# Kernel tuning notes

Hardware: AMD Instinct MI355X
Metric: run time of the kernel (lower is better)

## Reference

```python
import jax, jax.numpy as jnp
import numpy as np


def setup_inputs() -> dict:
    key = jax.random.key(0)
    k1, k2 = jax.random.split(key)
    preds = jax.random.normal(k1, (16, 4096, 3), dtype=jnp.float32)
    gts = jax.random.normal(k2, (16, 4096, 3), dtype=jnp.float32)
    return {"preds": preds, "gts": gts}


def _pairwise_sqdist(x, y):
    # x: [B, N1, D], y: [B, N2, D] -> P: [B, N1, N2]
    rx = jnp.sum(x * x, axis=-1)  # [B, N1]
    ry = jnp.sum(y * y, axis=-1)  # [B, N2]
    zz = jnp.einsum("bnd,bmd->bnm", x, y)  # [B, N1, N2]
    return rx[:, :, None] + ry[:, None, :] - 2.0 * zz


def reference(preds, gts):
    # Symmetric Hausdorff distance (squared-dist version) per batch element.
    P = _pairwise_sqdist(preds, gts)  # [B, N1, N2]
    # min over preds (axis 1) for each gt point, then max over gt points
    loss1 = jnp.max(jnp.min(P, axis=1), axis=1)  # [B]
    # min over gts (axis 2) for each pred point, then max over pred points
    loss2 = jnp.max(jnp.min(P, axis=2), axis=1)  # [B]
    return (loss1 + loss2) * 0.5
```

## Files before the change

kernel.cpp:

```cpp
#include <hip/hip_runtime.h>
#include <math.h>


#define NPTS 4096
#define NB 16
#define TPB 256
#define M 8
#define SPLIT 16
#define HT (TPB * M)
#define OC (NPTS / SPLIT)
#define NHT (NPTS / HT)

#define WSMIN_N (2 * NB * NPTS)

__global__ __launch_bounds__(TPB) void haus_scan_kernel(
        const float* __restrict__ preds, const float* __restrict__ gts,
        unsigned int* __restrict__ wsmin) {
    const int ht  = blockIdx.x & (NHT - 1);
    const int oc  = blockIdx.x >> 1;
    const int b   = blockIdx.y;
    const int dir = blockIdx.z;
    const int t   = threadIdx.x;

    const float* home = (dir == 0) ? gts : preds;
    const float* opp  = (dir == 0) ? preds : gts;
    const float* hb = home + (size_t)b * NPTS * 3;
    const float* ob = opp  + (size_t)b * NPTS * 3;

    __shared__ float4 q[OC];
    {
        const float* src = ob + (size_t)(oc * OC + t) * 3;
        float qx = src[0], qy = src[1], qz = src[2];
        float hq = 0.5f * fmaf(qx, qx, fmaf(qy, qy, qz * qz));
        q[t] = make_float4(qx, qy, qz, hq);
    }

    float px[M], py[M], pz[M], best[M];
#pragma unroll
    for (int k = 0; k < M; ++k) {
        int hi = ht * HT + k * TPB + t;
        px[k] = hb[hi * 3 + 0];
        py[k] = hb[hi * 3 + 1];
        pz[k] = hb[hi * 3 + 2];
        best[k] = INFINITY;
    }

    __syncthreads();

#pragma unroll 4
    for (int j = 0; j < OC; ++j) {
        float4 q4 = q[j];
        float qx = q4.x, qy = q4.y, qz = q4.z, qw = q4.w;
        asm("" : "+v"(qx), "+v"(qy), "+v"(qz), "+v"(qw));
#pragma unroll
        for (int k = 0; k < M; ++k) {
            float acc = fmaf(-px[k], qx, qw);
            acc = fmaf(-py[k], qy, acc);
            acc = fmaf(-pz[k], qz, acc);
            best[k] = fminf(best[k], acc);
        }
    }

    unsigned int* slot = wsmin + ((size_t)dir * NB + b) * NPTS;
#pragma unroll
    for (int k = 0; k < M; ++k) {
        int hi = ht * HT + k * TPB + t;
        float hp = 0.5f * fmaf(px[k], px[k], fmaf(py[k], py[k], pz[k] * pz[k]));
        float d2 = fmaxf(best[k] + hp, 0.0f);
        atomicMin(slot + hi, __float_as_uint(d2));
    }
}

__global__ __launch_bounds__(TPB) void haus_final_kernel(
        const unsigned int* __restrict__ wsmin, float* __restrict__ out) {
    const int b = blockIdx.x;
    const int t = threadIdx.x;
    const float4* w0 = (const float4*)(wsmin + ((size_t)0 * NB + b) * NPTS);
    const float4* w1 = (const float4*)(wsmin + ((size_t)1 * NB + b) * NPTS);
    float m1 = -INFINITY, m2 = -INFINITY;
#pragma unroll
    for (int r = 0; r < NPTS / 4 / TPB; ++r) {
        float4 a = w0[r * TPB + t];
        float4 c = w1[r * TPB + t];
        m1 = fmaxf(fmaxf(fmaxf(a.x, a.y), fmaxf(a.z, a.w)), m1);
        m2 = fmaxf(fmaxf(fmaxf(c.x, c.y), fmaxf(c.z, c.w)), m2);
    }
#pragma unroll
    for (int off = 32; off > 0; off >>= 1) {
        m1 = fmaxf(m1, __shfl_down(m1, off, 64));
        m2 = fmaxf(m2, __shfl_down(m2, off, 64));
    }
    __shared__ float s1[4], s2[4];
    if ((t & 63) == 0) { s1[t >> 6] = m1; s2[t >> 6] = m2; }
    __syncthreads();
    if (t == 0) {
        float a = fmaxf(fmaxf(s1[0], s1[1]), fmaxf(s1[2], s1[3]));
        float c = fmaxf(fmaxf(s2[0], s2[1]), fmaxf(s2[2], s2[3]));
        out[b] = a + c;
    }
}

extern "C" void kernel_launch(void* const* d_in, const int* in_sizes, int n_in,
                              void* d_out, int out_size, void* d_ws, size_t ws_size,
                              hipStream_t stream) {
    const float* preds = (const float*)d_in[0];
    const float* gts   = (const float*)d_in[1];
    float* out = (float*)d_out;
    unsigned int* wsmin = (unsigned int*)d_ws;

    hipMemsetAsync(wsmin, 0xFF, (size_t)WSMIN_N * sizeof(unsigned int), stream);

    haus_scan_kernel<<<dim3(NHT * SPLIT, NB, 2), dim3(TPB), 0, stream>>>(
        preds, gts, wsmin);

    haus_final_kernel<<<dim3(NB), dim3(TPB), 0, stream>>>(wsmin, out);
}
```

Baseline: 97.54 us.

## Use packed v_pk_fma_f32 and give each thread 16 home points

The inner distance loop now pairs two home points per register and computes their partial distances with v_pk_fma_f32 inline assembly. This cuts the FMA instruction count per pair roughly in half, while the fmin stays scalar. Each thread now holds 16 home points, so one block covers all 4096 points in a batch. The opposite set is split 32 ways with 128 points per block, so each LDS query load is reused across more points. Register use goes up, and the hand-written op_sel encodings must match the intended lane selection.

After: 95.71 us. No clear change (-1.9%).

```diff
diff --git a/kernel.cpp b/kernel.cpp
--- a/kernel.cpp
+++ b/kernel.cpp
@@ -5,19 +5,19 @@
 #define NPTS 4096
 #define NB 16
 #define TPB 256
-#define M 8
-#define SPLIT 16
-#define HT (TPB * M)
+#define M 16
+#define MP (M / 2)
+#define SPLIT 32
 #define OC (NPTS / SPLIT)
-#define NHT (NPTS / HT)
 
 #define WSMIN_N (2 * NB * NPTS)
+
+typedef float v2f __attribute__((ext_vector_type(2)));
 
 __global__ __launch_bounds__(TPB) void haus_scan_kernel(
         const float* __restrict__ preds, const float* __restrict__ gts,
         unsigned int* __restrict__ wsmin) {
-    const int ht  = blockIdx.x & (NHT - 1);
-    const int oc  = blockIdx.x >> 1;
+    const int oc  = blockIdx.x;
     const int b   = blockIdx.y;
     const int dir = blockIdx.z;
     const int t   = threadIdx.x;
@@ -27,47 +27,59 @@
     const float* hb = home + (size_t)b * NPTS * 3;
     const float* ob = opp  + (size_t)b * NPTS * 3;
 
-    __shared__ float4 q[OC];
-    {
+    __shared__ v2f sxy[OC], szh[OC];
+    if (t < OC) {
         const float* src = ob + (size_t)(oc * OC + t) * 3;
         float qx = src[0], qy = src[1], qz = src[2];
         float hq = 0.5f * fmaf(qx, qx, fmaf(qy, qy, qz * qz));
-        q[t] = make_float4(qx, qy, qz, hq);
+        sxy[t] = (v2f){qx, qy};
+        szh[t] = (v2f){qz, hq};
     }
 
-    float px[M], py[M], pz[M], best[M];
+    v2f phx[MP], phy[MP], phz[MP], best2[MP];
 #pragma unroll
-    for (int k = 0; k < M; ++k) {
-        int hi = ht * HT + k * TPB + t;
-        px[k] = hb[hi * 3 + 0];
-        py[k] = hb[hi * 3 + 1];
-        pz[k] = hb[hi * 3 + 2];
-        best[k] = INFINITY;
+    for (int kp = 0; kp < MP; ++kp) {
+        int ha = (2 * kp) * TPB + t;
+        int hb_i = (2 * kp + 1) * TPB + t;
+        phx[kp] = (v2f){-hb[ha * 3 + 0], -hb[hb_i * 3 + 0]};
+        phy[kp] = (v2f){-hb[ha * 3 + 1], -hb[hb_i * 3 + 1]};
+        phz[kp] = (v2f){-hb[ha * 3 + 2], -hb[hb_i * 3 + 2]};
+        best2[kp] = (v2f){INFINITY, INFINITY};
     }
 
     __syncthreads();
 
-#pragma unroll 4
+#pragma unroll 2
     for (int j = 0; j < OC; ++j) {
-        float4 q4 = q[j];
-        float qx = q4.x, qy = q4.y, qz = q4.z, qw = q4.w;
-        asm("" : "+v"(qx), "+v"(qy), "+v"(qz), "+v"(qw));
+        v2f qxy = sxy[j];
+        v2f qzh = szh[j];
 #pragma unroll
-        for (int k = 0; k < M; ++k) {
-            float acc = fmaf(-px[k], qx, qw);
-            acc = fmaf(-py[k], qy, acc);
-            acc = fmaf(-pz[k], qz, acc);
-            best[k] = fminf(best[k], acc);
+        for (int kp = 0; kp < MP; ++kp) {
+            v2f acc;
+            asm("v_pk_fma_f32 %0, %1, %2, %3 op_sel:[0,0,1] op_sel_hi:[1,0,1]"
+                : "=v"(acc) : "v"(phx[kp]), "v"(qxy), "v"(qzh));
+            asm("v_pk_fma_f32 %0, %1, %2, %0 op_sel:[0,1,0] op_sel_hi:[1,1,1]"
+                : "+v"(acc) : "v"(phy[kp]), "v"(qxy));
+            asm("v_pk_fma_f32 %0, %1, %2, %0 op_sel:[0,0,0] op_sel_hi:[1,0,1]"
+                : "+v"(acc) : "v"(phz[kp]), "v"(qzh));
+            best2[kp][0] = fminf(best2[kp][0], acc[0]);
+            best2[kp][1] = fminf(best2[kp][1], acc[1]);
         }
     }
 
     unsigned int* slot = wsmin + ((size_t)dir * NB + b) * NPTS;
 #pragma unroll
-    for (int k = 0; k < M; ++k) {
-        int hi = ht * HT + k * TPB + t;
-        float hp = 0.5f * fmaf(px[k], px[k], fmaf(py[k], py[k], pz[k] * pz[k]));
-        float d2 = fmaxf(best[k] + hp, 0.0f);
-        atomicMin(slot + hi, __float_as_uint(d2));
+    for (int kp = 0; kp < MP; ++kp) {
+        int ha = (2 * kp) * TPB + t;
+        int hb_i = (2 * kp + 1) * TPB + t;
+        float xa = phx[kp][0], ya = phy[kp][0], za = phz[kp][0];
+        float xb = phx[kp][1], yb = phy[kp][1], zb = phz[kp][1];
+        float hpa = 0.5f * fmaf(xa, xa, fmaf(ya, ya, za * za));
+        float hpb = 0.5f * fmaf(xb, xb, fmaf(yb, yb, zb * zb));
+        float da = fmaxf(best2[kp][0] + hpa, 0.0f);
+        float db = fmaxf(best2[kp][1] + hpb, 0.0f);
+        atomicMin(slot + ha, __float_as_uint(da));
+        atomicMin(slot + hb_i, __float_as_uint(db));
     }
 }
 
@@ -110,7 +122,7 @@
 
     hipMemsetAsync(wsmin, 0xFF, (size_t)WSMIN_N * sizeof(unsigned int), stream);
 
-    haus_scan_kernel<<<dim3(NHT * SPLIT, NB, 2), dim3(TPB), 0, stream>>>(
+    haus_scan_kernel<<<dim3(SPLIT, NB, 2), dim3(TPB), 0, stream>>>(
         preds, gts, wsmin);
 
     haus_final_kernel<<<dim3(NB), dim3(TPB), 0, stream>>>(wsmin, out);
```

## Compute pairwise distances with split-fp16 MFMA instead of scalar FMA loop

Applied to the files above, without the earlier changes.

Replaces the scalar FMA distance scan with 32x32x16 fp16 MFMA tiles. Each fp32 coordinate is split into high and low fp16 parts so the dot product plus the squared norm of the opposite point is approximately recovered in fp32 accumulation. Row minima are reduced with cross-lane shuffles and written through atomicMin, and the grid is re-split to 128 home points per block and 4 opposite chunks. The split representation keeps extra precision but drops the low-times-low cross terms and rounds the norm to two fp16 parts, so accuracy is slightly reduced. The final kernel now applies the 0.5 factor to the summed maxima because the new distances use full squared norms.

New measurement: 93.30 us. -4.3%, faster.

```diff
diff --git a/kernel.cpp b/kernel.cpp
--- a/kernel.cpp
+++ b/kernel.cpp
@@ -5,69 +5,113 @@
 #define NPTS 4096
 #define NB 16
 #define TPB 256
-#define M 8
-#define SPLIT 16
-#define HT (TPB * M)
-#define OC (NPTS / SPLIT)
-#define NHT (NPTS / HT)
+#define WAVES 4
+#define HPW 32
+#define HPB (WAVES * HPW)
+#define NHB (NPTS / HPB)
+#define SPLIT 4
+#define OPP (NPTS / SPLIT)
+#define TILES (OPP / 32)
 
 #define WSMIN_N (2 * NB * NPTS)
+
+typedef _Float16 h8 __attribute__((ext_vector_type(8)));
+typedef float f16v __attribute__((ext_vector_type(16)));
 
 __global__ __launch_bounds__(TPB) void haus_scan_kernel(
         const float* __restrict__ preds, const float* __restrict__ gts,
         unsigned int* __restrict__ wsmin) {
-    const int ht  = blockIdx.x & (NHT - 1);
-    const int oc  = blockIdx.x >> 1;
+    const int hb  = blockIdx.x & (NHB - 1);
+    const int sp  = blockIdx.x >> 5;
     const int b   = blockIdx.y;
     const int dir = blockIdx.z;
     const int t   = threadIdx.x;
+    const int lane = t & 63, w = t >> 6;
+    const int l31 = lane & 31, half = lane >> 5;
 
     const float* home = (dir == 0) ? gts : preds;
     const float* opp  = (dir == 0) ? preds : gts;
-    const float* hb = home + (size_t)b * NPTS * 3;
-    const float* ob = opp  + (size_t)b * NPTS * 3;
+    const float* hbp = home + (size_t)b * NPTS * 3;
+    const float* obp = opp  + (size_t)b * NPTS * 3;
 
-    __shared__ float4 q[OC];
-    {
-        const float* src = ob + (size_t)(oc * OC + t) * 3;
-        float qx = src[0], qy = src[1], qz = src[2];
-        float hq = 0.5f * fmaf(qx, qx, fmaf(qy, qy, qz * qz));
-        q[t] = make_float4(qx, qy, qz, hq);
+    __shared__ h8 srec[2 * OPP];
+    __shared__ float shg[WAVES][HPW];
+
+    for (int i = 0; i < OPP / TPB; ++i) {
+        int p = i * TPB + t;
+        const float* s = obp + (size_t)(sp * OPP + p) * 3;
+        float x = s[0], y = s[1], z = s[2];
+        float hp = fmaf(x, x, fmaf(y, y, z * z));
+        _Float16 xh = (_Float16)x, yh = (_Float16)y, zh = (_Float16)z;
+        _Float16 xl = (_Float16)(x - (float)xh);
+        _Float16 yl = (_Float16)(y - (float)yh);
+        _Float16 zl = (_Float16)(z - (float)zh);
+        _Float16 hph = (_Float16)hp, hpl = (_Float16)(hp - (float)hph);
+        h8 lo, hi;
+        lo[0] = xh; lo[1] = yh; lo[2] = zh;
+        lo[3] = xl; lo[4] = yl; lo[5] = zl;
+        lo[6] = xh; lo[7] = yh;
+        hi[0] = zh;
+        hi[1] = hph; hi[2] = hpl;
+        hi[3] = (_Float16)0; hi[4] = (_Float16)0;
+        hi[5] = (_Float16)0; hi[6] = (_Float16)0; hi[7] = (_Float16)0;
+        srec[p] = lo;
+        srec[OPP + p] = hi;
     }
 
-    float px[M], py[M], pz[M], best[M];
+    int m = hb * HPB + w * HPW + l31;
+    float gx = hbp[m * 3 + 0], gy = hbp[m * 3 + 1], gz = hbp[m * 3 + 2];
+    float hg = fmaf(gx, gx, fmaf(gy, gy, gz * gz));
+    shg[w][l31] = hg;
+    _Float16 gxh = (_Float16)gx, gyh = (_Float16)gy, gzh = (_Float16)gz;
+    _Float16 gxl = (_Float16)(gx - (float)gxh);
+    _Float16 gyl = (_Float16)(gy - (float)gyh);
+    _Float16 gzl = (_Float16)(gz - (float)gzh);
+    const _Float16 n2 = (_Float16)(-2.0f);
+    h8 afrag;
+    if (half == 0) {
+        afrag[0] = n2 * gxh; afrag[1] = n2 * gyh; afrag[2] = n2 * gzh;
+        afrag[3] = n2 * gxh; afrag[4] = n2 * gyh; afrag[5] = n2 * gzh;
+        afrag[6] = n2 * gxl; afrag[7] = n2 * gyl;
+    } else {
+        afrag[0] = n2 * gzl;
+        afrag[1] = (_Float16)1; afrag[2] = (_Float16)1;
+        afrag[3] = (_Float16)0; afrag[4] = (_Float16)0;
+        afrag[5] = (_Float16)0; afrag[6] = (_Float16)0; afrag[7] = (_Float16)0;
+    }
+
+    f16v zc = {};
+    float best[16];
 #pragma unroll
-    for (int k = 0; k < M; ++k) {
-        int hi = ht * HT + k * TPB + t;
-        px[k] = hb[hi * 3 + 0];
-        py[k] = hb[hi * 3 + 1];
-        pz[k] = hb[hi * 3 + 2];
-        best[k] = INFINITY;
-    }
+    for (int r = 0; r < 16; ++r) best[r] = INFINITY;
 
     __syncthreads();
 
-#pragma unroll 4
-    for (int j = 0; j < OC; ++j) {
-        float4 q4 = q[j];
-        float qx = q4.x, qy = q4.y, qz = q4.z, qw = q4.w;
-        asm("" : "+v"(qx), "+v"(qy), "+v"(qz), "+v"(qw));
+    const int base = half * OPP + l31;
+#pragma unroll 2
+    for (int tt = 0; tt < TILES; ++tt) {
+        h8 bfrag = srec[base + tt * 32];
+        f16v D = __builtin_amdgcn_mfma_f32_32x32x16_f16(afrag, bfrag, zc, 0, 0, 0);
 #pragma unroll
-        for (int k = 0; k < M; ++k) {
-            float acc = fmaf(-px[k], qx, qw);
-            acc = fmaf(-py[k], qy, acc);
-            acc = fmaf(-pz[k], qz, acc);
-            best[k] = fminf(best[k], acc);
-        }
+        for (int r = 0; r < 16; ++r) best[r] = fminf(best[r], D[r]);
     }
 
-    unsigned int* slot = wsmin + ((size_t)dir * NB + b) * NPTS;
 #pragma unroll
-    for (int k = 0; k < M; ++k) {
-        int hi = ht * HT + k * TPB + t;
-        float hp = 0.5f * fmaf(px[k], px[k], fmaf(py[k], py[k], pz[k] * pz[k]));
-        float d2 = fmaxf(best[k] + hp, 0.0f);
-        atomicMin(slot + hi, __float_as_uint(d2));
+    for (int off = 16; off >= 1; off >>= 1) {
+#pragma unroll
+        for (int r = 0; r < 16; ++r)
+            best[r] = fminf(best[r], __shfl_xor(best[r], off, 64));
+    }
+
+    unsigned int* slot = wsmin + ((size_t)dir * NB + b) * NPTS + hb * HPB + w * HPW;
+    if (l31 == 0) {
+#pragma unroll
+        for (int r = 0; r < 16; ++r) {
+            int row = (r & 3) + 8 * (r >> 2) + 4 * half;
+            float d = best[r] + shg[w][row];
+            d = fmaxf(d, 0.0f);
+            atomicMin(slot + row, __float_as_uint(d));
+        }
     }
 }
 
@@ -96,7 +140,7 @@
     if (t == 0) {
         float a = fmaxf(fmaxf(s1[0], s1[1]), fmaxf(s1[2], s1[3]));
         float c = fmaxf(fmaxf(s2[0], s2[1]), fmaxf(s2[2], s2[3]));
-        out[b] = a + c;
+        out[b] = 0.5f * (a + c);
     }
 }
 
@@ -110,7 +154,7 @@
 
     hipMemsetAsync(wsmin, 0xFF, (size_t)WSMIN_N * sizeof(unsigned int), stream);
 
-    haus_scan_kernel<<<dim3(NHT * SPLIT, NB, 2), dim3(TPB), 0, stream>>>(
+    haus_scan_kernel<<<dim3(NHB * SPLIT, NB, 2), dim3(TPB), 0, stream>>>(
         preds, gts, wsmin);
 
     haus_final_kernel<<<dim3(NB), dim3(TPB), 0, stream>>>(wsmin, out);
```
